# Kernel tuning notes

Hardware: AMD Instinct MI355X
Metric: run time of the kernel (lower is better)

Reference implementation:

```python
import jax, jax.numpy as jnp
import numpy as np

T, N, NH, H, R, E = 6, 50000, 128, 4, 2, 800000
D = NH // H


def _pos_enc(d, t):
    # matches HTHGNLayer TempAttention.generate_positional_encoding
    k = np.arange(0, d, 2)
    div = np.exp(k * -np.log(100000.0) / d)
    pos = np.arange(1, t + 1)[:, None].astype(np.float64)
    pe = np.zeros((t, d), dtype=np.float32)
    pe[:, 0::2] = np.sin(pos * div)
    pe[:, 1::2] = np.cos(pos * div)
    return jnp.asarray(pe)


def setup_inputs() -> dict:
    key = jax.random.key(0)
    ks = jax.random.split(key, 16)
    s = 1.0 / np.sqrt(NH)  # keep activations / attention logits well-scaled
    inp = {
        "x": jax.random.normal(ks[0], (T, N, NH), jnp.float32),
        "src": jax.random.randint(ks[1], (R, E), 0, N, jnp.int32),
        "dst": jax.random.randint(ks[2], (R, E), 0, N, jnp.int32),
        "gat_wsrc": jax.random.normal(ks[3], (R, NH, NH), jnp.float32) * s,
        "gat_wdst": jax.random.normal(ks[4], (R, NH, NH), jnp.float32) * s,
        "gat_attn": jax.random.normal(ks[5], (R, H, D), jnp.float32) * s,
        "gat_bias": jnp.zeros((R, NH), jnp.float32),
        "h_bias": jnp.zeros((NH,), jnp.float32),
        "sem_w1": jax.random.normal(ks[6], (NH, NH), jnp.float32) * s,
        "sem_b1": jnp.zeros((NH,), jnp.float32),
        "sem_w2": jax.random.normal(ks[7], (NH,), jnp.float32) * s,
        "proj_w": jax.random.normal(ks[8], (NH, NH), jnp.float32) * s,
        "proj_b": jnp.zeros((NH,), jnp.float32),
        "qw": jax.random.normal(ks[9], (NH, NH), jnp.float32) * s,
        "kw": jax.random.normal(ks[10], (NH, NH), jnp.float32) * s,
        "vw": jax.random.normal(ks[11], (NH, NH), jnp.float32) * s,
        "fc_w": jax.random.normal(ks[12], (NH, NH), jnp.float32) * s,
        "fc_b": jnp.zeros((NH,), jnp.float32),
        "res_w": jax.random.normal(ks[13], (NH, NH), jnp.float32) * s,
        "res_b": jnp.zeros((NH,), jnp.float32),
        "res_alpha": jax.random.normal(ks[14], (1,), jnp.float32),
        "ln_gamma": jnp.ones((NH,), jnp.float32),
        "ln_beta": jnp.zeros((NH,), jnp.float32),
    }
    return inp


def _gatv2_rel(xt, s_, d_, wsrc, wdst, attn, bias):
    # one relation, one timestep: DGL GATv2Conv (share_weights=False, slope 0.2)
    fs = (xt @ wsrc).reshape(N, H, D)  # fc_src
    fd = (xt @ wdst).reshape(N, H, D)  # fc_dst
    e = jax.nn.leaky_relu(fs[s_] + fd[d_], 0.2)           # [E,H,D]
    sc = jnp.einsum('ehd,hd->eh', e, attn)                # [E,H]
    m = jax.ops.segment_max(sc, d_, num_segments=N)       # edge softmax per dst
    ex = jnp.exp(sc - m[d_])
    den = jax.ops.segment_sum(ex, d_, num_segments=N)
    alpha = ex / den[d_]
    out = jax.ops.segment_sum(alpha[:, :, None] * fs[s_], d_, num_segments=N)
    return out + bias.reshape(1, H, D)                    # [N,H,D]


def reference(x, src, dst, gat_wsrc, gat_wdst, gat_attn, gat_bias, h_bias,
              sem_w1, sem_b1, sem_w2, proj_w, proj_b, qw, kw, vw, fc_w, fc_b,
              res_w, res_b, res_alpha, ln_gamma, ln_beta):
    gat_all = jax.vmap(_gatv2_rel, in_axes=(None, 0, 0, 0, 0, 0, 0))
    inter = []
    for t in range(T):  # fixed small time window
        hr = gat_all(x[t], src, dst, gat_wsrc, gat_wdst, gat_attn, gat_bias)  # [R,N,H,D]
        h = jnp.transpose(hr, (1, 0, 2, 3)).reshape(N, R, NH)  # stack + flatten heads
        # semantic attention over relations (_rel_agg)
        w = jnp.tanh(h @ sem_w1 + sem_b1) @ sem_w2             # [N,R]
        beta = jax.nn.softmax(w.mean(0), axis=0)               # [R]
        hsem = jax.nn.relu(jnp.einsum('r,nrd->nd', beta, h))
        inter.append(jax.nn.relu(hsem + h_bias))               # _apply: bias + relu
    inter = jnp.stack(inter, 0)                                # [T,N,NH]
    # temporal self-attention (TempAttention, no 1/sqrt(d) scaling -- faithful)
    pe = _pos_enc(NH, T)
    xt = jnp.transpose(inter, (1, 0, 2))                       # [N,T,NH]
    hh = xt @ proj_w + proj_b + pe
    q, k, v = hh @ qw, hh @ kw, hh @ vw
    sc = jax.nn.softmax(jnp.einsum('ntd,nsd->nts', q, k), axis=-1)
    ho = jax.nn.relu(jnp.einsum('nts,nsd->ntd', sc, v) @ fc_w + fc_b)
    ho = jnp.transpose(ho, (1, 0, 2))                          # [T,N,NH]
    # gated residual + LayerNorm
    a = jax.nn.sigmoid(res_alpha)[0]
    out = ho * a + (x @ res_w + res_b) * (1.0 - a)
    mu = out.mean(-1, keepdims=True)
    var = out.var(-1, keepdims=True)
    return (out - mu) / jnp.sqrt(var + 1e-5) * ln_gamma + ln_beta
```

## Files before the change

### kernel.cpp

```cpp
#include <hip/hip_runtime.h>
#include <math.h>

#define T_  6
#define N_  50000
#define NH_ 128
#define R_  2
#define E_  800000
#define SEMW_BLOCKS ((2*N_ + 127)/128)
#define NCHUNK 49

typedef __attribute__((ext_vector_type(8))) short bf16x8;
typedef __attribute__((ext_vector_type(4))) float f32x4;

__device__ inline unsigned short f2b(float f) {
    union { float f; unsigned int u; } v; v.f = f;
    unsigned int u = v.u;
    unsigned int r = (u + 0x7FFFu + ((u >> 16) & 1u)) >> 16;
    return (unsigned short)r;
}
__device__ inline float b2f(unsigned short h) {
    union { unsigned int u; float f; } v; v.u = ((unsigned int)h) << 16;
    return v.f;
}

__global__ void hist_kernel(const int* __restrict__ dst, int* __restrict__ counts) {
    int j = blockIdx.x * blockDim.x + threadIdx.x;
    if (j < R_ * E_) atomicAdd(&counts[(j / E_) * N_ + dst[j]], 1);
}

__global__ __launch_bounds__(1024) void scan1_kernel(const int* __restrict__ counts,
                                                     int* __restrict__ lexcl,
                                                     int* __restrict__ csums) {
    int r = blockIdx.y, c = blockIdx.x;
    int i = c * 1024 + threadIdx.x;
    int v = (i < N_) ? counts[r * N_ + i] : 0;
    __shared__ int sm[1024];
    sm[threadIdx.x] = v;
    __syncthreads();
    for (int off = 1; off < 1024; off <<= 1) {
        int t = 0;
        if (threadIdx.x >= off) t = sm[threadIdx.x - off];
        __syncthreads();
        sm[threadIdx.x] += t;
        __syncthreads();
    }
    if (i < N_) lexcl[r * N_ + i] = sm[threadIdx.x] - v;
    if (threadIdx.x == 1023) csums[r * 64 + c] = sm[1023];
}

__global__ void scan2_kernel(int* __restrict__ csums, int* __restrict__ offsets) {
    int r = threadIdx.x >> 6, l = threadIdx.x & 63;
    if (r < R_) {
        int v = (l < NCHUNK) ? csums[r * 64 + l] : 0;
        int s = v;
        for (int off = 1; off < 64; off <<= 1) {
            int t = __shfl_up(s, off);
            if (l >= off) s += t;
        }
        if (l < NCHUNK) csums[r * 64 + l] = s - v;
        if (l == NCHUNK - 1) offsets[r * (N_ + 1) + N_] = s;
    }
}

__global__ __launch_bounds__(1024) void scan3_kernel(const int* __restrict__ lexcl,
                                                     const int* __restrict__ csums,
                                                     int* __restrict__ offsets,
                                                     int* __restrict__ cursor) {
    int r = blockIdx.y;
    int i = blockIdx.x * 1024 + threadIdx.x;
    if (i < N_) {
        int o = lexcl[r * N_ + i] + csums[r * 64 + blockIdx.x];
        offsets[r * (N_ + 1) + i] = o;
        cursor[r * N_ + i] = o;
    }
}

__global__ void scatter_kernel(const int* __restrict__ src, const int* __restrict__ dst,
                               int* __restrict__ cursor, int* __restrict__ srcs_sorted) {
    int j = blockIdx.x * blockDim.x + threadIdx.x;
    if (j < R_ * E_) {
        int r = j / E_;
        int pos = atomicAdd(&cursor[r * N_ + dst[j]], 1);
        srcs_sorted[(size_t)r * E_ + pos] = src[j] << 8;
    }
}

__global__ void pe_kernel(float* __restrict__ pe) {
    int c = threadIdx.x;
    int k = c & ~1;
    double div = exp((double)k * (-log(100000.0) / 128.0));
    for (int t = 0; t < T_; t++) {
        double pos = (double)(t + 1);
        double v = (c & 1) ? cos(pos * div) : sin(pos * div);
        pe[t * NH_ + c] = (float)v;
    }
}

__global__ void cvt_x_kernel(const float* __restrict__ in, unsigned short* __restrict__ out, long n) {
    long i = ((long)blockIdx.x * blockDim.x + threadIdx.x) * 8;
    if (i >= n) return;
    float4 a = *(const float4*)(in + i);
    float4 b = *(const float4*)(in + i + 4);
    union { unsigned short s[8]; uint4 u; } o;
    o.s[0] = f2b(a.x); o.s[1] = f2b(a.y); o.s[2] = f2b(a.z); o.s[3] = f2b(a.w);
    o.s[4] = f2b(b.x); o.s[5] = f2b(b.y); o.s[6] = f2b(b.z); o.s[7] = f2b(b.w);
    *(uint4*)(out + i) = o.u;
}

struct CvtArgs {
    const float* s[6];
    unsigned short* d[6];
};
__global__ void cvt_wt_kernel(CvtArgs a) {
    int y = blockIdx.y, n = blockIdx.x, k = threadIdx.x;
    a.d[y][n * 128 + k] = f2b(a.s[y][k * 128 + n]);
}

__global__ void build_m_kernel(const float* __restrict__ qw, const float* __restrict__ kw,
                               const float* __restrict__ vw, const float* __restrict__ fcw,
                               float* __restrict__ Mu, float* __restrict__ Mwv) {
    int y = blockIdx.y, c = blockIdx.x, f = threadIdx.x;
    float s = 0.f;
    if (y == 0) {
        for (int d = 0; d < 128; d++) s += kw[f * 128 + d] * qw[c * 128 + d];
        Mu[c * 128 + f] = s;
    } else {
        for (int d = 0; d < 128; d++) s += vw[f * 128 + d] * fcw[d * 128 + c];
        Mwv[c * 128 + f] = s;
    }
}

__global__ void fold_w_kernel(const float* __restrict__ proj, const float* __restrict__ Mu,
                              const float* __restrict__ Mwv, unsigned short* __restrict__ wt_hh,
                              unsigned short* __restrict__ wt_pu, unsigned short* __restrict__ wt_pwv) {
    int y = blockIdx.y, c = blockIdx.x, k = threadIdx.x;
    if (y == 0) { wt_hh[c * 128 + k] = f2b(proj[k * 128 + c]); return; }
    const float* M = (y == 1) ? Mu : Mwv;
    float s = 0.f;
    for (int f = 0; f < 128; f++) s += proj[k * 128 + f] * M[c * 128 + f];
    ((y == 1) ? wt_pu : wt_pwv)[c * 128 + k] = f2b(s);
}

__global__ void fold_c_kernel(const float* __restrict__ proj_b, const float* __restrict__ pe,
                              const float* __restrict__ Mu, const float* __restrict__ Mwv,
                              const float* __restrict__ res_b, float* __restrict__ cbuf) {
    int t = blockIdx.x, c = threadIdx.x;
    cbuf[0 * 768 + t * 128 + c] = proj_b[c] + pe[t * 128 + c];
    float s1 = 0.f, s2 = 0.f;
    for (int f = 0; f < 128; f++) {
        float b = proj_b[f] + pe[t * 128 + f];
        s1 += b * Mu[c * 128 + f];
        s2 += b * Mwv[c * 128 + f];
    }
    cbuf[1 * 768 + t * 128 + c] = s1;
    cbuf[2 * 768 + t * 128 + c] = s2;
    cbuf[3 * 768 + t * 128 + c] = res_b[c];
}

struct MArgs {
    const unsigned short* A;
    const unsigned short* Axb;
    const unsigned short* W0; const unsigned short* W1;
    const unsigned short* W2; const unsigned short* W3;
    unsigned short* C0; unsigned short* C1; unsigned short* C2; unsigned short* C3;
    const float* cb;
    long row0;
    int  M;
};

template <int EPI>
__global__ __launch_bounds__(256) void mgemm_kernel(MArgs g) {
    __shared__ __align__(16) char As[128 * 256];
    __shared__ __align__(16) char Bs[128 * 256];
    int tid = threadIdx.x;
    int brow0 = blockIdx.x * 128;
    const unsigned short* Ws[4] = {g.W0, g.W1, g.W2, g.W3};
    unsigned short* Cs[4] = {g.C0, g.C1, g.C2, g.C3};

    auto stageA = [&](const unsigned short* Abase, bool m1) {
#pragma unroll
        for (int i = 0; i < 8; i++) {
            int c = tid + i * 256;
            int row = c >> 4;
            int cb = (c & 15) << 4;
            int scb = cb ^ ((row & 7) << 4);
            int grow = brow0 + row;
            float4 av = make_float4(0.f, 0.f, 0.f, 0.f);
            if (grow < g.M) {
                long ar;
                if (!m1) ar = grow;
                else { long gg = g.row0 + grow; long n = gg / 6, t = gg - n * 6; ar = t * (long)N_ + n; }
                av = *(const float4*)((const char*)Abase + ar * 256 + cb);
            }
            *(float4*)(As + row * 256 + scb) = av;
        }
    };
    auto stageB = [&](const unsigned short* W) {
#pragma unroll
        for (int i = 0; i < 8; i++) {
            int c = tid + i * 256;
            int row = c >> 4;
            int cb = (c & 15) << 4;
            int scb = cb ^ ((row & 7) << 4);
            *(float4*)(Bs + row * 256 + scb) = *(const float4*)((const char*)W + (size_t)row * 256 + cb);
        }
    };

    int w = tid >> 6, l = tid & 63;
    int l15 = l & 15, lg = l >> 4;

    stageA(g.A, false);
    for (int y = 0; y < 4; y++) {
        if (y > 0) __syncthreads();
        if (EPI == 3 && y == 3) stageA(g.Axb, true);
        stageB(Ws[y]);
        __syncthreads();

        f32x4 acc[2][8];
#pragma unroll
        for (int a = 0; a < 2; a++)
#pragma unroll
            for (int b = 0; b < 8; b++) acc[a][b] = (f32x4)(0.f);
#pragma unroll
        for (int ks = 0; ks < 4; ks++) {
            bf16x8 bf[8];
#pragma unroll
            for (int nt = 0; nt < 8; nt++) {
                int rn = nt * 16 + l15;
                int cbyte = (ks * 64 + lg * 16) ^ ((rn & 7) << 4);
                bf[nt] = *(const bf16x8*)(Bs + rn * 256 + cbyte);
            }
#pragma unroll
            for (int mt = 0; mt < 2; mt++) {
                int rm = w * 32 + mt * 16 + l15;
                int cbyte = (ks * 64 + lg * 16) ^ ((rm & 7) << 4);
                bf16x8 af = *(const bf16x8*)(As + rm * 256 + cbyte);
#pragma unroll
                for (int nt = 0; nt < 8; nt++)
                    acc[mt][nt] = __builtin_amdgcn_mfma_f32_16x16x32_bf16(af, bf[nt], acc[mt][nt], 0, 0, 0);
            }
        }
        unsigned short* C = Cs[y];
#pragma unroll
        for (int mt = 0; mt < 2; mt++) {
#pragma unroll
            for (int r = 0; r < 4; r++) {
                int row = w * 32 + mt * 16 + lg * 4 + r;
                int grow = brow0 + row;
                if (grow >= g.M) continue;
                long t6 = 0;
                if (EPI == 3) t6 = (g.row0 + grow) % 6;
#pragma unroll
                for (int nt = 0; nt < 8; nt++) {
                    int col = nt * 16 + l15;
                    float v = acc[mt][nt][r];
                    if (EPI == 3) v += g.cb[y * 768 + t6 * 128 + col];
                    C[(size_t)grow * 128 + col] = f2b(v);
                }
            }
        }
    }
}

__global__ __launch_bounds__(256) void semw_kernel(const unsigned short* __restrict__ Abase,
                                                   const unsigned short* __restrict__ Wt,
                                                   const float* __restrict__ b1,
                                                   const float* __restrict__ w2,
                                                   float* __restrict__ partials) {
    __shared__ __align__(16) char As[128 * 256];
    __shared__ __align__(16) char Bs[128 * 256];
    __shared__ float bs[2];
    int tid = threadIdx.x;
    if (tid < 2) bs[tid] = 0.f;
    int tl = blockIdx.y;
    const unsigned short* A = Abase + (size_t)tl * N_ * 256;
    const int M = 2 * N_;
    int brow0 = blockIdx.x * 128;
#pragma unroll
    for (int i = 0; i < 8; i++) {
        int c = tid + i * 256;
        int row = c >> 4;
        int cb = (c & 15) << 4;
        int scb = cb ^ ((row & 7) << 4);
        *(float4*)(Bs + row * 256 + scb) = *(const float4*)((const char*)Wt + (size_t)row * 256 + cb);
        int grow = brow0 + row;
        float4 av = make_float4(0.f, 0.f, 0.f, 0.f);
        if (grow < M) av = *(const float4*)((const char*)A + (size_t)grow * 256 + cb);
        *(float4*)(As + row * 256 + scb) = av;
    }
    __syncthreads();
    int w = tid >> 6, l = tid & 63;
    int l15 = l & 15, lg = l >> 4;
    f32x4 acc[2][8];
#pragma unroll
    for (int a = 0; a < 2; a++)
#pragma unroll
        for (int b = 0; b < 8; b++) acc[a][b] = (f32x4)(0.f);
#pragma unroll
    for (int ks = 0; ks < 4; ks++) {
        bf16x8 bf[8];
#pragma unroll
        for (int nt = 0; nt < 8; nt++) {
            int rn = nt * 16 + l15;
            int cbyte = (ks * 64 + lg * 16) ^ ((rn & 7) << 4);
            bf[nt] = *(const bf16x8*)(Bs + rn * 256 + cbyte);
        }
#pragma unroll
        for (int mt = 0; mt < 2; mt++) {
            int rm = w * 32 + mt * 16 + l15;
            int cbyte = (ks * 64 + lg * 16) ^ ((rm & 7) << 4);
            bf16x8 af = *(const bf16x8*)(As + rm * 256 + cbyte);
#pragma unroll
            for (int nt = 0; nt < 8; nt++)
                acc[mt][nt] = __builtin_amdgcn_mfma_f32_16x16x32_bf16(af, bf[nt], acc[mt][nt], 0, 0, 0);
        }
    }
#pragma unroll
    for (int mt = 0; mt < 2; mt++) {
#pragma unroll
        for (int r = 0; r < 4; r++) {
            int row = w * 32 + mt * 16 + lg * 4 + r;
            int grow = brow0 + row;
            float s = 0.f;
#pragma unroll
            for (int nt = 0; nt < 8; nt++) {
                int col = nt * 16 + l15;
                s += tanhf(acc[mt][nt][r] + b1[col]) * w2[col];
            }
#pragma unroll
            for (int mask = 1; mask <= 8; mask <<= 1) s += __shfl_xor(s, mask);
            if (l15 == 0 && grow < M) atomicAdd(&bs[grow & 1], s);
        }
    }
    __syncthreads();
    if (tid < 2) partials[((size_t)tl * SEMW_BLOCKS + blockIdx.x) * 2 + tid] = bs[tid];
}

__global__ __launch_bounds__(512) void beta_kernel(const float* __restrict__ partials,
                                                   float* __restrict__ beta2) {
    int t = blockIdx.x;
    const float* p = partials + (size_t)t * SEMW_BLOCKS * 2;
    float s0 = 0.f, s1 = 0.f;
    for (int i = threadIdx.x; i < SEMW_BLOCKS; i += 512) { s0 += p[i * 2]; s1 += p[i * 2 + 1]; }
#pragma unroll
    for (int mask = 1; mask <= 32; mask <<= 1) { s0 += __shfl_xor(s0, mask); s1 += __shfl_xor(s1, mask); }
    __shared__ float w0[8], w1[8];
    int w = threadIdx.x >> 6;
    if ((threadIdx.x & 63) == 0) { w0[w] = s0; w1[w] = s1; }
    __syncthreads();
    if (threadIdx.x == 0) {
        float t0 = 0.f, t1 = 0.f;
        for (int i = 0; i < 8; i++) { t0 += w0[i]; t1 += w1[i]; }
        float m0 = t0 / (float)N_, m1 = t1 / (float)N_;
        float mx = fmaxf(m0, m1);
        float e0 = __expf(m0 - mx), e1 = __expf(m1 - mx);
        float inv = 1.f / (e0 + e1);
        beta2[t * 2] = e0 * inv; beta2[t * 2 + 1] = e1 * inv;
    }
}

__global__ __launch_bounds__(256) void gat_edge_kernel(const unsigned short* __restrict__ R0,
                                                       const int* __restrict__ offsets,
                                                       const int* __restrict__ srcs_sorted,
                                                       const float* __restrict__ gat_attn,
                                                       const float* __restrict__ gat_bias,
                                                       unsigned short* __restrict__ hbuf, int TB) {
    int y = blockIdx.y;
    int r = y & 1, tl = y >> 1;
    const char* fsb = (const char*)(R0 + ((size_t)(2 * r) * TB + tl) * N_ * 128);
    const unsigned short* fd = R0 + ((size_t)(2 * r + 1) * TB + tl) * N_ * 128;
    unsigned short* hout = hbuf + (size_t)tl * N_ * 256;
    const int* offs = offsets + r * (N_ + 1);
    const int* srcs = srcs_sorted + (size_t)r * E_;
    int lane = threadIdx.x & 63;
    int q = lane >> 4, l16 = lane & 15;
    int c0 = l16 * 8;
    const char* fsc = fsb + c0 * 2;
    int wid = (blockIdx.x * blockDim.x + threadIdx.x) >> 6;
    int nw = (gridDim.x * blockDim.x) >> 6;
    float4 a0 = *(const float4*)(gat_attn + r * 128 + c0);
    float4 a1 = *(const float4*)(gat_attn + r * 128 + c0 + 4);
    float av[8] = {a0.x, a0.y, a0.z, a0.w, a1.x, a1.y, a1.z, a1.w};
    float4 bb0 = *(const float4*)(gat_bias + r * 128 + c0);
    float4 bb1 = *(const float4*)(gat_bias + r * 128 + c0 + 4);
    float bv[8] = {bb0.x, bb0.y, bb0.z, bb0.w, bb1.x, bb1.y, bb1.z, bb1.w};

    for (int gidx = wid; gidx < N_ / 4; gidx += nw) {
        int n = gidx * 4 + q;
        uint4 fdp = *(const uint4*)(fd + (size_t)n * 128 + c0);
        const unsigned int* fdu = (const unsigned int*)&fdp;
        float fdv[8];
#pragma unroll
        for (int j = 0; j < 8; j++)
            fdv[j] = (j & 1) ? b2f((unsigned short)(fdu[j >> 1] >> 16)) : b2f((unsigned short)fdu[j >> 1]);
        int e0 = offs[n], e1 = offs[n + 1];
        int deg = e1 - e0;
        int m = deg;
        m = max(m, __shfl_xor(m, 16));
        m = max(m, __shfl_xor(m, 32));
        float den = 0.f;
        float acc[8];
#pragma unroll
        for (int j = 0; j < 8; j++) acc[j] = 0.f;

        uint4 fp = make_uint4(0, 0, 0, 0);
        if (deg > 0) fp = *(const uint4*)(fsc + srcs[e0]);
        for (int i = 0; i < m; i++) {
            uint4 nxt = make_uint4(0, 0, 0, 0);
            if (i + 1 < deg) nxt = *(const uint4*)(fsc + srcs[e0 + i + 1]);
            const unsigned int* fu = (const unsigned int*)&fp;
            float f[8];
            float vlin = 0.f, vabs = 0.f;
#pragma unroll
            for (int j = 0; j < 8; j++) {
                f[j] = (j & 1) ? b2f((unsigned short)(fu[j >> 1] >> 16)) : b2f((unsigned short)fu[j >> 1]);
                float t = f[j] + fdv[j];
                vlin = fmaf(av[j], t, vlin);
                vabs = fmaf(av[j], fabsf(t), vabs);
            }
            vlin += __int_as_float(__builtin_amdgcn_ds_swizzle(__float_as_int(vlin), 0x041F));
            vabs += __int_as_float(__builtin_amdgcn_ds_swizzle(__float_as_int(vabs), 0x041F));
            vlin += __int_as_float(__builtin_amdgcn_ds_swizzle(__float_as_int(vlin), 0x081F));
            vabs += __int_as_float(__builtin_amdgcn_ds_swizzle(__float_as_int(vabs), 0x081F));
            float v = fmaf(0.4f, vabs, 0.6f * vlin);
            float p = (i < deg) ? __expf(v) : 0.f;
            den += p;
#pragma unroll
            for (int j = 0; j < 8; j++) acc[j] = fmaf(p, f[j], acc[j]);
            fp = nxt;
        }
        float inv = (deg > 0) ? 1.f / den : 0.f;
        union { unsigned short s[8]; uint4 u; } o;
#pragma unroll
        for (int j = 0; j < 8; j++) o.s[j] = f2b(fmaf(acc[j], inv, bv[j]));
        *(uint4*)(hout + (size_t)(n * 2 + r) * 128 + c0) = o.u;
    }
}

__global__ void hsem_kernel(const unsigned short* __restrict__ hbuf, const float* __restrict__ beta2,
                            const float* __restrict__ h_bias, unsigned short* __restrict__ inter,
                            int tbase) {
    int idx = blockIdx.x * blockDim.x + threadIdx.x;
    if (idx >= N_ * 16) return;
    int tl = blockIdx.y;
    int t = tbase + tl;
    const unsigned short* h = hbuf + (size_t)tl * N_ * 256;
    int n = idx >> 4, c8 = (idx & 15) * 8;
    float b0 = beta2[tl * 2], b1 = beta2[tl * 2 + 1];
    uint4 x0 = *(const uint4*)(h + (size_t)n * 256 + c8);
    uint4 x1 = *(const uint4*)(h + (size_t)n * 256 + 128 + c8);
    const unsigned int* p0 = (const unsigned int*)&x0;
    const unsigned int* p1 = (const unsigned int*)&x1;
    float4 hb0 = *(const float4*)(h_bias + c8);
    float4 hb1 = *(const float4*)(h_bias + c8 + 4);
    float hbv[8] = {hb0.x, hb0.y, hb0.z, hb0.w, hb1.x, hb1.y, hb1.z, hb1.w};
    union { unsigned short s[8]; uint4 u; } o;
#pragma unroll
    for (int i = 0; i < 8; i++) {
        unsigned short s0 = (i & 1) ? (unsigned short)(p0[i >> 1] >> 16) : (unsigned short)p0[i >> 1];
        unsigned short s1 = (i & 1) ? (unsigned short)(p1[i >> 1] >> 16) : (unsigned short)p1[i >> 1];
        float z = fmaxf(fmaxf(b0 * b2f(s0) + b1 * b2f(s1), 0.f) + hbv[i], 0.f);
        o.s[i] = f2b(z);
    }
    *(uint4*)(inter + ((size_t)n * 6 + t) * 128 + c8) = o.u;
}

__global__ __launch_bounds__(256) void temporal_kernel(const unsigned short* __restrict__ hh,
                                                       const unsigned short* __restrict__ uu,
                                                       const unsigned short* __restrict__ wvv,
                                                       const unsigned short* __restrict__ rv,
                                                       const float* __restrict__ fc_b,
                                                       const float* __restrict__ res_alpha,
                                                       const float* __restrict__ ln_g,
                                                       const float* __restrict__ ln_b,
                                                       float* __restrict__ out, long n0, int nNodes) {
    int lane = threadIdx.x & 63;
    int wid = (blockIdx.x * blockDim.x + threadIdx.x) >> 6;
    if (wid >= nNodes) return;
    long n = n0 + wid;
    size_t base = (size_t)wid * 6 * 128 + 2 * lane;
    float h2[6][2], u2[6][2], wv2[6][2], rv2[6][2];
#pragma unroll
    for (int t = 0; t < 6; t++) {
        unsigned int hp = *(const unsigned int*)(hh + base + t * 128);
        h2[t][0] = b2f((unsigned short)hp); h2[t][1] = b2f((unsigned short)(hp >> 16));
        unsigned int up = *(const unsigned int*)(uu + base + t * 128);
        u2[t][0] = b2f((unsigned short)up); u2[t][1] = b2f((unsigned short)(up >> 16));
        unsigned int wp = *(const unsigned int*)(wvv + base + t * 128);
        wv2[t][0] = b2f((unsigned short)wp); wv2[t][1] = b2f((unsigned short)(wp >> 16));
        unsigned int rp = *(const unsigned int*)(rv + base + t * 128);
        rv2[t][0] = b2f((unsigned short)rp); rv2[t][1] = b2f((unsigned short)(rp >> 16));
    }
    float sc[6][6];
#pragma unroll
    for (int t = 0; t < 6; t++)
#pragma unroll
        for (int s = 0; s < 6; s++)
            sc[t][s] = h2[t][0] * u2[s][0] + h2[t][1] * u2[s][1];
#pragma unroll
    for (int mask = 1; mask <= 32; mask <<= 1)
#pragma unroll
        for (int t = 0; t < 6; t++)
#pragma unroll
            for (int s = 0; s < 6; s++)
                sc[t][s] += __shfl_xor(sc[t][s], mask);

    float a = 1.f / (1.f + __expf(-res_alpha[0]));
    float2 fb = ((const float2*)fc_b)[lane];
    float2 lg = ((const float2*)ln_g)[lane];
    float2 lb = ((const float2*)ln_b)[lane];
#pragma unroll
    for (int t = 0; t < 6; t++) {
        float mx = sc[t][0];
#pragma unroll
        for (int s = 1; s < 6; s++) mx = fmaxf(mx, sc[t][s]);
        float p[6]; float den = 0.f;
#pragma unroll
        for (int s = 0; s < 6; s++) { p[s] = __expf(sc[t][s] - mx); den += p[s]; }
        float inv = 1.f / den;
        float ox = 0.f, oy = 0.f;
#pragma unroll
        for (int s = 0; s < 6; s++) { ox += p[s] * wv2[s][0]; oy += p[s] * wv2[s][1]; }
        ox = fmaxf(ox * inv + fb.x, 0.f);
        oy = fmaxf(oy * inv + fb.y, 0.f);
        ox = ox * a + rv2[t][0] * (1.f - a);
        oy = oy * a + rv2[t][1] * (1.f - a);
        float s1 = ox + oy, s2 = ox * ox + oy * oy;
#pragma unroll
        for (int mask = 1; mask <= 32; mask <<= 1) {
            s1 += __shfl_xor(s1, mask);
            s2 += __shfl_xor(s2, mask);
        }
        float mu = s1 * (1.f / 128.f);
        float var = s2 * (1.f / 128.f) - mu * mu;
        float rs = rsqrtf(var + 1e-5f);
        float2 o;
        o.x = (ox - mu) * rs * lg.x + lb.x;
        o.y = (oy - mu) * rs * lg.y + lb.y;
        ((float2*)(out + ((size_t)t * N_ + n) * 128))[lane] = o;
    }
}

extern "C" void kernel_launch(void* const* d_in, const int* in_sizes, int n_in,
                              void* d_out, int out_size, void* d_ws, size_t ws_size,
                              hipStream_t stream) {
    const float* x        = (const float*)d_in[0];
    const int*   src      = (const int*)d_in[1];
    const int*   dst      = (const int*)d_in[2];
    const float* gat_wsrc = (const float*)d_in[3];
    const float* gat_wdst = (const float*)d_in[4];
    const float* gat_attn = (const float*)d_in[5];
    const float* gat_bias = (const float*)d_in[6];
    const float* h_bias   = (const float*)d_in[7];
    const float* sem_w1   = (const float*)d_in[8];
    const float* sem_b1   = (const float*)d_in[9];
    const float* sem_w2   = (const float*)d_in[10];
    const float* proj_w   = (const float*)d_in[11];
    const float* proj_b   = (const float*)d_in[12];
    const float* qw       = (const float*)d_in[13];
    const float* kw       = (const float*)d_in[14];
    const float* vw       = (const float*)d_in[15];
    const float* fc_w     = (const float*)d_in[16];
    const float* fc_b     = (const float*)d_in[17];
    const float* res_w    = (const float*)d_in[18];
    const float* res_b    = (const float*)d_in[19];
    const float* res_alpha= (const float*)d_in[20];
    const float* ln_g     = (const float*)d_in[21];
    const float* ln_b     = (const float*)d_in[22];
    (void)in_sizes; (void)n_in; (void)out_size;

    int TB = (ws_size >= (size_t)500 * 1024 * 1024) ? 6 : 2;
    int CH = (TB == 6) ? N_ : 12500;

    char* ws = (char*)d_ws;
    size_t off = 0;
    auto alloc = [&](size_t bytes) -> void* {
        void* p = ws + off;
        off += (bytes + 255) & ~(size_t)255;
        return p;
    };
    int*   counts      = (int*)alloc((size_t)R_ * N_ * 4);
    int*   offsets     = (int*)alloc((size_t)R_ * (N_ + 1) * 4);
    int*   cursor      = (int*)alloc((size_t)R_ * N_ * 4);
    int*   srcs_sorted = (int*)alloc((size_t)R_ * E_ * 4);
    int*   lexcl       = (int*)alloc((size_t)R_ * N_ * 4);
    int*   csums       = (int*)alloc((size_t)R_ * 64 * 4);
    float* pe          = (float*)alloc(T_ * NH_ * 4);
    float* partials    = (float*)alloc((size_t)T_ * SEMW_BLOCKS * 2 * 4);
    float* beta2       = (float*)alloc(T_ * 2 * 4);
    float* Mu          = (float*)alloc(16384 * 4);
    float* Mwv         = (float*)alloc(16384 * 4);
    float* cbuf        = (float*)alloc(4 * 768 * 4);
    unsigned short* wt_gs0  = (unsigned short*)alloc(16384 * 2);
    unsigned short* wt_gs1  = (unsigned short*)alloc(16384 * 2);
    unsigned short* wt_gd0  = (unsigned short*)alloc(16384 * 2);
    unsigned short* wt_gd1  = (unsigned short*)alloc(16384 * 2);
    unsigned short* wt_sem  = (unsigned short*)alloc(16384 * 2);
    unsigned short* wt_res  = (unsigned short*)alloc(16384 * 2);
    unsigned short* wt_hh   = (unsigned short*)alloc(16384 * 2);
    unsigned short* wt_pu   = (unsigned short*)alloc(16384 * 2);
    unsigned short* wt_pwv  = (unsigned short*)alloc(16384 * 2);
    unsigned short* xb      = (unsigned short*)alloc((size_t)T_ * N_ * 128 * 2);
    unsigned short* inter   = (unsigned short*)alloc((size_t)N_ * T_ * 128 * 2);
    size_t Rgat = (size_t)4 * TB * N_ * 128 * 2;
    size_t Rtmp = (size_t)4 * CH * 6 * 128 * 2;
    unsigned short* R0      = (unsigned short*)alloc(Rgat > Rtmp ? Rgat : Rtmp);

    unsigned short* hbuf = (unsigned short*)d_out;

    hipMemsetAsync(counts, 0, (size_t)R_ * N_ * 4, stream);
    hist_kernel<<<(R_ * E_ + 255) / 256, 256, 0, stream>>>(dst, counts);
    scan1_kernel<<<dim3(NCHUNK, R_), 1024, 0, stream>>>(counts, lexcl, csums);
    scan2_kernel<<<1, 128, 0, stream>>>(csums, offsets);
    scan3_kernel<<<dim3(NCHUNK, R_), 1024, 0, stream>>>(lexcl, csums, offsets, cursor);
    scatter_kernel<<<(R_ * E_ + 255) / 256, 256, 0, stream>>>(src, dst, cursor, srcs_sorted);
    pe_kernel<<<1, 128, 0, stream>>>(pe);
    cvt_x_kernel<<<18750, 256, 0, stream>>>(x, xb, (long)T_ * N_ * 128);
    CvtArgs ca;
    ca.s[0] = gat_wsrc;         ca.d[0] = wt_gs0;
    ca.s[1] = gat_wsrc + 16384; ca.d[1] = wt_gs1;
    ca.s[2] = gat_wdst;         ca.d[2] = wt_gd0;
    ca.s[3] = gat_wdst + 16384; ca.d[3] = wt_gd1;
    ca.s[4] = sem_w1;           ca.d[4] = wt_sem;
    ca.s[5] = res_w;            ca.d[5] = wt_res;
    cvt_wt_kernel<<<dim3(128, 6), 128, 0, stream>>>(ca);
    build_m_kernel<<<dim3(128, 2), 128, 0, stream>>>(qw, kw, vw, fc_w, Mu, Mwv);
    fold_w_kernel<<<dim3(128, 3), 128, 0, stream>>>(proj_w, Mu, Mwv, wt_hh, wt_pu, wt_pwv);
    fold_c_kernel<<<6, 128, 0, stream>>>(proj_b, pe, Mu, Mwv, res_b, cbuf);

    size_t TBN = (size_t)TB * N_ * 128;
    for (int tg = 0; tg < T_ / TB; tg++) {
        int tbase = tg * TB;
        MArgs ga{};
        ga.A = xb + (size_t)tbase * N_ * 128;
        ga.row0 = 0; ga.M = TB * N_;
        ga.W0 = wt_gs0; ga.C0 = R0;
        ga.W1 = wt_gd0; ga.C1 = R0 + TBN;
        ga.W2 = wt_gs1; ga.C2 = R0 + 2 * TBN;
        ga.W3 = wt_gd1; ga.C3 = R0 + 3 * TBN;
        mgemm_kernel<0><<<dim3((TB * N_ + 127) / 128, 1), 256, 0, stream>>>(ga);

        gat_edge_kernel<<<dim3(1024, 2 * TB), 256, 0, stream>>>(R0, offsets, srcs_sorted,
                                                                gat_attn, gat_bias, hbuf, TB);

        semw_kernel<<<dim3(SEMW_BLOCKS, TB), 256, 0, stream>>>(hbuf, wt_sem, sem_b1, sem_w2,
                                                               partials + (size_t)tbase * SEMW_BLOCKS * 2);
        beta_kernel<<<TB, 512, 0, stream>>>(partials + (size_t)tbase * SEMW_BLOCKS * 2,
                                            beta2 + tbase * 2);
        hsem_kernel<<<dim3((N_ * 16 + 255) / 256, TB), 256, 0, stream>>>(hbuf, beta2 + tbase * 2,
                                                                         h_bias, inter, tbase);
    }

    for (int c = 0; c < N_ / CH; c++) {
        long n0 = (long)c * CH;
        long r0 = n0 * 6;
        int Mc = CH * 6;
        int nb = (Mc + 127) / 128;
        size_t MB = (size_t)Mc * 128;

        MArgs gt{};
        gt.A = inter + (size_t)r0 * 128;
        gt.Axb = xb;
        gt.row0 = r0; gt.M = Mc; gt.cb = cbuf;
        gt.W0 = wt_hh;  gt.C0 = R0;
        gt.W1 = wt_pu;  gt.C1 = R0 + MB;
        gt.W2 = wt_pwv; gt.C2 = R0 + 2 * MB;
        gt.W3 = wt_res; gt.C3 = R0 + 3 * MB;
        mgemm_kernel<3><<<dim3(nb, 1), 256, 0, stream>>>(gt);

        temporal_kernel<<<(CH + 3) / 4, 256, 0, stream>>>(R0, R0 + MB, R0 + 2 * MB, R0 + 3 * MB,
                                                          fc_b, res_alpha, ln_g, ln_b,
                                                          (float*)d_out, n0, CH);
    }
}
```

Before: 1.336 ms.

## Fuse fp32-to-bf16 conversion of x into GEMM A-tile staging; merge swizzle reductions

Drops the standalone cvt_x kernel and its bf16 copy of x. The GEMMs now read fp32 x directly and convert to bf16 while staging A tiles into shared memory. This removes one full pass that wrote x back out as bf16, at the cost of twice the bytes per A-tile load in the GEMMs. The edge kernel also combines vlin and vabs into one value before the cross-lane swizzle reduction, halving the swizzles.

```diff
diff --git a/kernel.cpp b/kernel.cpp
--- a/kernel.cpp
+++ b/kernel.cpp
@@ -96,17 +96,6 @@
     }
 }
 
-__global__ void cvt_x_kernel(const float* __restrict__ in, unsigned short* __restrict__ out, long n) {
-    long i = ((long)blockIdx.x * blockDim.x + threadIdx.x) * 8;
-    if (i >= n) return;
-    float4 a = *(const float4*)(in + i);
-    float4 b = *(const float4*)(in + i + 4);
-    union { unsigned short s[8]; uint4 u; } o;
-    o.s[0] = f2b(a.x); o.s[1] = f2b(a.y); o.s[2] = f2b(a.z); o.s[3] = f2b(a.w);
-    o.s[4] = f2b(b.x); o.s[5] = f2b(b.y); o.s[6] = f2b(b.z); o.s[7] = f2b(b.w);
-    *(uint4*)(out + i) = o.u;
-}
-
 struct CvtArgs {
     const float* s[6];
     unsigned short* d[6];
@@ -158,8 +147,8 @@
 }
 
 struct MArgs {
-    const unsigned short* A;
-    const unsigned short* Axb;
+    const void* A;
+    const void* Axb;
     const unsigned short* W0; const unsigned short* W1;
     const unsigned short* W2; const unsigned short* W3;
     unsigned short* C0; unsigned short* C1; unsigned short* C2; unsigned short* C3;
@@ -177,7 +166,7 @@
     const unsigned short* Ws[4] = {g.W0, g.W1, g.W2, g.W3};
     unsigned short* Cs[4] = {g.C0, g.C1, g.C2, g.C3};
 
-    auto stageA = [&](const unsigned short* Abase, bool m1) {
+    auto stageA = [&](const void* Abase, bool m1, bool f32src) {
 #pragma unroll
         for (int i = 0; i < 8; i++) {
             int c = tid + i * 256;
@@ -185,14 +174,24 @@
             int cb = (c & 15) << 4;
             int scb = cb ^ ((row & 7) << 4);
             int grow = brow0 + row;
-            float4 av = make_float4(0.f, 0.f, 0.f, 0.f);
+            uint4 av = make_uint4(0u, 0u, 0u, 0u);
             if (grow < g.M) {
                 long ar;
                 if (!m1) ar = grow;
                 else { long gg = g.row0 + grow; long n = gg / 6, t = gg - n * 6; ar = t * (long)N_ + n; }
-                av = *(const float4*)((const char*)Abase + ar * 256 + cb);
+                if (f32src) {
+                    const float* Af = (const float*)Abase + ar * 128 + (cb >> 1);
+                    float4 x0 = *(const float4*)Af;
+                    float4 x1 = *(const float4*)(Af + 4);
+                    union { unsigned short s[8]; uint4 u; } o;
+                    o.s[0] = f2b(x0.x); o.s[1] = f2b(x0.y); o.s[2] = f2b(x0.z); o.s[3] = f2b(x0.w);
+                    o.s[4] = f2b(x1.x); o.s[5] = f2b(x1.y); o.s[6] = f2b(x1.z); o.s[7] = f2b(x1.w);
+                    av = o.u;
+                } else {
+                    av = *(const uint4*)((const char*)Abase + ar * 256 + cb);
+                }
             }
-            *(float4*)(As + row * 256 + scb) = av;
+            *(uint4*)(As + row * 256 + scb) = av;
         }
     };
     auto stageB = [&](const unsigned short* W) {
@@ -209,10 +208,10 @@
     int w = tid >> 6, l = tid & 63;
     int l15 = l & 15, lg = l >> 4;
 
-    stageA(g.A, false);
+    stageA(g.A, false, EPI == 0);
     for (int y = 0; y < 4; y++) {
         if (y > 0) __syncthreads();
-        if (EPI == 3 && y == 3) stageA(g.Axb, true);
+        if (EPI == 3 && y == 3) stageA(g.Axb, true, true);
         stageB(Ws[y]);
         __syncthreads();
 
@@ -403,10 +402,10 @@
 #pragma unroll
         for (int j = 0; j < 8; j++) acc[j] = 0.f;
 
-        uint4 fp = make_uint4(0, 0, 0, 0);
+        uint4 fp = make_uint4(0u, 0u, 0u, 0u);
         if (deg > 0) fp = *(const uint4*)(fsc + srcs[e0]);
         for (int i = 0; i < m; i++) {
-            uint4 nxt = make_uint4(0, 0, 0, 0);
+            uint4 nxt = make_uint4(0u, 0u, 0u, 0u);
             if (i + 1 < deg) nxt = *(const uint4*)(fsc + srcs[e0 + i + 1]);
             const unsigned int* fu = (const unsigned int*)&fp;
             float f[8];
@@ -418,11 +417,9 @@
                 vlin = fmaf(av[j], t, vlin);
                 vabs = fmaf(av[j], fabsf(t), vabs);
             }
-            vlin += __int_as_float(__builtin_amdgcn_ds_swizzle(__float_as_int(vlin), 0x041F));
-            vabs += __int_as_float(__builtin_amdgcn_ds_swizzle(__float_as_int(vabs), 0x041F));
-            vlin += __int_as_float(__builtin_amdgcn_ds_swizzle(__float_as_int(vlin), 0x081F));
-            vabs += __int_as_float(__builtin_amdgcn_ds_swizzle(__float_as_int(vabs), 0x081F));
             float v = fmaf(0.4f, vabs, 0.6f * vlin);
+            v += __int_as_float(__builtin_amdgcn_ds_swizzle(__float_as_int(v), 0x041F));
+            v += __int_as_float(__builtin_amdgcn_ds_swizzle(__float_as_int(v), 0x081F));
             float p = (i < deg) ? __expf(v) : 0.f;
             den += p;
 #pragma unroll
@@ -600,7 +597,6 @@
     unsigned short* wt_hh   = (unsigned short*)alloc(16384 * 2);
     unsigned short* wt_pu   = (unsigned short*)alloc(16384 * 2);
     unsigned short* wt_pwv  = (unsigned short*)alloc(16384 * 2);
-    unsigned short* xb      = (unsigned short*)alloc((size_t)T_ * N_ * 128 * 2);
     unsigned short* inter   = (unsigned short*)alloc((size_t)N_ * T_ * 128 * 2);
     size_t Rgat = (size_t)4 * TB * N_ * 128 * 2;
     size_t Rtmp = (size_t)4 * CH * 6 * 128 * 2;
@@ -615,7 +611,6 @@
     scan3_kernel<<<dim3(NCHUNK, R_), 1024, 0, stream>>>(lexcl, csums, offsets, cursor);
     scatter_kernel<<<(R_ * E_ + 255) / 256, 256, 0, stream>>>(src, dst, cursor, srcs_sorted);
     pe_kernel<<<1, 128, 0, stream>>>(pe);
-    cvt_x_kernel<<<18750, 256, 0, stream>>>(x, xb, (long)T_ * N_ * 128);
     CvtArgs ca;
     ca.s[0] = gat_wsrc;         ca.d[0] = wt_gs0;
     ca.s[1] = gat_wsrc + 16384; ca.d[1] = wt_gs1;
@@ -632,7 +627,7 @@
     for (int tg = 0; tg < T_ / TB; tg++) {
         int tbase = tg * TB;
         MArgs ga{};
-        ga.A = xb + (size_t)tbase * N_ * 128;
+        ga.A = (const void*)(x + (size_t)tbase * N_ * 128);
         ga.row0 = 0; ga.M = TB * N_;
         ga.W0 = wt_gs0; ga.C0 = R0;
         ga.W1 = wt_gd0; ga.C1 = R0 + TBN;
@@ -659,8 +654,8 @@
         size_t MB = (size_t)Mc * 128;
 
         MArgs gt{};
-        gt.A = inter + (size_t)r0 * 128;
-        gt.Axb = xb;
+        gt.A = (const void*)(inter + (size_t)r0 * 128);
+        gt.Axb = (const void*)x;
         gt.row0 = r0; gt.M = Mc; gt.cb = cbuf;
         gt.W0 = wt_hh;  gt.C0 = R0;
         gt.W1 = wt_pu;  gt.C1 = R0 + MB;
```

After: 1.311 ms. About the same (-1.9%).
